# Optimization experiments

Hardware: AMD Instinct MI355X
Metric: run time of the kernel (lower is better)

## Reference

```python
import jax, jax.numpy as jnp
import numpy as np

D_MODEL = 512
HEADS = 8
D_FF = 1024
EPS = 1e-5


def layer_norm(x, gamma, beta):
    mu = jnp.mean(x, axis=-1, keepdims=True)
    var = jnp.mean(jnp.square(x - mu), axis=-1, keepdims=True)
    return (x - mu) * jax.lax.rsqrt(var + EPS) * gamma + beta


def mha(q, k, v, mask=None):
    # q,k,v: [B, S, D]; no input/output projections in the original module
    B, Sq, D = q.shape
    Sk = k.shape[1]
    dk = D // HEADS
    qh = q.reshape(B, Sq, HEADS, dk).transpose(0, 2, 1, 3)  # [B,H,Sq,dk]
    kh = k.reshape(B, Sk, HEADS, dk).transpose(0, 2, 1, 3)
    vh = v.reshape(B, Sk, HEADS, dk).transpose(0, 2, 1, 3)
    scores = jnp.einsum('bhqd,bhkd->bhqk', qh, kh) / np.sqrt(dk).astype(q.dtype)
    if mask is not None:
        scores = jnp.where(mask == 0, jnp.asarray(-1e9, scores.dtype), scores)
    attn = jax.nn.softmax(scores, axis=-1)  # dropout is identity in eval mode
    out = jnp.einsum('bhqk,bhkd->bhqd', attn, vh)
    return out.transpose(0, 2, 1, 3).reshape(B, Sq, D)


def setup_inputs() -> dict:
    key = jax.random.key(0)
    ks = jax.random.split(key, 8)
    B, S = 4, 2048
    x = jax.random.normal(ks[0], (B, S, D_MODEL), dtype=jnp.float32)
    encoder_output = jax.random.normal(ks[1], (B, S, D_MODEL), dtype=jnp.float32)
    mask = jax.random.randint(ks[2], (B, 1, S, S), 0, 2, dtype=jnp.int32)
    params = {
        'ln1_g': jnp.ones((D_MODEL,), jnp.float32), 'ln1_b': jnp.zeros((D_MODEL,), jnp.float32),
        'ln2_g': jnp.ones((D_MODEL,), jnp.float32), 'ln2_b': jnp.zeros((D_MODEL,), jnp.float32),
        'ln3_g': jnp.ones((D_MODEL,), jnp.float32), 'ln3_b': jnp.zeros((D_MODEL,), jnp.float32),
        'W1': jax.random.normal(ks[3], (D_MODEL, D_FF), jnp.float32) * (1.0 / np.sqrt(D_MODEL)),
        'b1': jnp.zeros((D_FF,), jnp.float32),
        'W2': jax.random.normal(ks[4], (D_FF, D_MODEL), jnp.float32) * (1.0 / np.sqrt(D_FF)),
        'b2': jnp.zeros((D_MODEL,), jnp.float32),
    }
    return {'x': x, 'encoder_output': encoder_output, 'mask': mask, **params}


def reference(x, encoder_output, mask, ln1_g, ln1_b, ln2_g, ln2_b, ln3_g, ln3_b, W1, b1, W2, b2):
    # pre-norm masked self-attention + residual (dropout = identity, eval mode)
    x1 = layer_norm(x, ln1_g, ln1_b)
    x = x + mha(x1, x1, x1, mask)
    # pre-norm cross-attention + residual
    x1 = layer_norm(x, ln2_g, ln2_b)
    x = x + mha(x1, encoder_output, encoder_output, None)
    # pre-norm FFN + residual
    x1 = layer_norm(x, ln3_g, ln3_b)
    h = jax.nn.relu(x1 @ W1 + b1)
    x = x + (h @ W2 + b2)
    return x
```

## Files before the change

### kernel.cpp

```cpp
#include <hip/hip_runtime.h>
#include <hip/hip_bf16.h>

#define D_MODEL 512
#define HEADS   8
#define DK      64
#define D_FF    1024
#define SEQ     2048
#define BATCH   4
#define NTOK    (BATCH*SEQ)
#define NELEM   (NTOK*D_MODEL)

#define QSCALE  0.18033688011112042f
#define MFIX    40.0f

typedef __attribute__((ext_vector_type(8))) short bf8_t;
typedef __attribute__((ext_vector_type(4))) short bf4_t;
typedef __attribute__((ext_vector_type(4))) float f4_t;

#define GLD16(gp, lp) __builtin_amdgcn_global_load_lds( \
    (const __attribute__((address_space(1))) void*)(gp), \
    (__attribute__((address_space(3))) void*)(lp), 16, 0, 0)

__device__ __forceinline__ float ldf(const void* p, size_t i, int f32) {
    return f32 ? ((const float*)p)[i] : __bfloat162float(((const __hip_bfloat16*)p)[i]);
}
__device__ __forceinline__ short f2bf(float f) {
    union { __hip_bfloat16 h; short s; } u; u.h = __float2bfloat16(f); return u.s;
}
__device__ __forceinline__ float bf2f(short s) {
    return __uint_as_float(((unsigned)(unsigned short)s) << 16);
}
__device__ __forceinline__ unsigned fbits(float f) { return __float_as_uint(f); }

__device__ __forceinline__ float fast_exp2(float x) {
    float r; asm("v_exp_f32 %0, %1" : "=v"(r) : "v"(x)); return r;
}

__global__ void detect_k(const uint4* __restrict__ w, int* __restrict__ flags) {
    __shared__ int found;
    if (threadIdx.x == 0) found = 0;
    __syncthreads();
    int hit = 0;
    for (int i = threadIdx.x; i < 4096; i += 256) {
        uint4 u = w[i];
        if (((u.x & 0x7F80u) == 0x7F80u) || ((u.y & 0x7F80u) == 0x7F80u) ||
            ((u.z & 0x7F80u) == 0x7F80u) || ((u.w & 0x7F80u) == 0x7F80u)) hit = 1;
    }
    if (hit) atomicOr(&found, 1);
    __syncthreads();
    if (threadIdx.x == 0) flags[0] = found ? 1 : 0;
}

__device__ __forceinline__ void transpose_body(const void* src, __hip_bfloat16* dst,
                                               int K, int N, int bxi, int byi, int f32,
                                               __hip_bfloat16 (*t)[33]) {
    int bx = bxi * 32, by = byi * 32;
    int tx = threadIdx.x & 31, ty = threadIdx.x >> 5;
    #pragma unroll
    for (int j = 0; j < 32; j += 8)
        t[ty + j][tx] = __float2bfloat16(ldf(src, (size_t)(by + ty + j) * N + bx + tx, f32));
    __syncthreads();
    #pragma unroll
    for (int j = 0; j < 32; j += 8)
        dst[(size_t)(bx + ty + j) * K + by + tx] = t[tx][ty + j];
}

__global__ __launch_bounds__(256)
void prep_k(const void* __restrict__ enc, const int* __restrict__ mask,
            const void* __restrict__ W1, const void* __restrict__ W2,
            const void* __restrict__ x,
            const void* __restrict__ ln1g, const void* __restrict__ ln1b,
            const void* __restrict__ ln2g, const void* __restrict__ ln2b,
            const void* __restrict__ ln3g, const void* __restrict__ ln3b,
            const void* __restrict__ b1,   const void* __restrict__ b2,
            const int* __restrict__ flagp,
            __hip_bfloat16* __restrict__ bufE, unsigned* __restrict__ mb,
            __hip_bfloat16* __restrict__ W1T, __hip_bfloat16* __restrict__ W2T,
            float* __restrict__ bufX, __hip_bfloat16* __restrict__ bufQ,
            __hip_bfloat16* __restrict__ pbuf) {
    __shared__ __hip_bfloat16 t[32][33];
    int f32 = *flagp;
    int bid = blockIdx.x;
    if (bid < 4096) {
        int i = bid * 256 + threadIdx.x;
        if (f32) {
            float4 a = ((const float4*)enc)[i];
            bf4_t o = { f2bf(a.x), f2bf(a.y), f2bf(a.z), f2bf(a.w) };
            ((bf4_t*)bufE)[i] = o;
        } else {
            ((bf4_t*)bufE)[i] = ((const bf4_t*)enc)[i];
        }
    } else if (bid < 6144) {
        int row  = (bid - 4096) * 4 + (threadIdx.x >> 6);
        int lane = threadIdx.x & 63;
        const int* mr = mask + (size_t)row * SEQ;
        for (int it = 0; it < SEQ/64; it++) {
            unsigned long long bal = __ballot(mr[it*64 + lane] != 0);
            if (lane == 0)  mb[(size_t)row*(SEQ/32) + it*2]     = (unsigned)bal;
            if (lane == 32) mb[(size_t)row*(SEQ/32) + it*2 + 1] = (unsigned)(bal >> 32);
        }
    } else if (bid < 6656) {
        int lb = bid - 6144;
        transpose_body(W1, W1T, D_MODEL, D_FF, lb & 31, lb >> 5, f32, t);
    } else if (bid < 7168) {
        int lb = bid - 6656;
        transpose_body(W2, W2T, D_FF, D_MODEL, lb & 15, lb >> 4, f32, t);
    } else if (bid < 9216) {
        int row  = (bid - 7168) * 4 + (threadIdx.x >> 6);
        int lane = threadIdx.x & 63;
        size_t base = (size_t)row * D_MODEL;
        float v[8];
        if (f32) {
            const float4* xp = (const float4*)((const float*)x + base);
            float4 a = xp[lane], b4 = xp[64 + lane];
            v[0]=a.x; v[1]=a.y; v[2]=a.z; v[3]=a.w;
            v[4]=b4.x; v[5]=b4.y; v[6]=b4.z; v[7]=b4.w;
        } else {
            const bf4_t* xp = (const bf4_t*)((const __hip_bfloat16*)x + base);
            bf4_t a = xp[lane], b4 = xp[64 + lane];
            v[0]=bf2f(a[0]); v[1]=bf2f(a[1]); v[2]=bf2f(a[2]); v[3]=bf2f(a[3]);
            v[4]=bf2f(b4[0]); v[5]=bf2f(b4[1]); v[6]=bf2f(b4[2]); v[7]=bf2f(b4[3]);
        }
        float s = 0.f;
        #pragma unroll
        for (int i = 0; i < 8; i++) s += v[i];
        #pragma unroll
        for (int off = 32; off; off >>= 1) s += __shfl_xor(s, off);
        float mu = s * (1.f / D_MODEL);
        float ss = 0.f;
        #pragma unroll
        for (int i = 0; i < 8; i++) { float d = v[i] - mu; ss += d * d; }
        #pragma unroll
        for (int off = 32; off; off >>= 1) ss += __shfl_xor(ss, off);
        float rstd = rsqrtf(ss * (1.f / D_MODEL) + 1e-5f);
        int c0 = 4*lane, c1 = 256 + 4*lane;
        ((float4*)(bufX + base))[lane]      = make_float4(v[0], v[1], v[2], v[3]);
        ((float4*)(bufX + base))[64 + lane] = make_float4(v[4], v[5], v[6], v[7]);
        bf4_t qa, qb;
        #pragma unroll
        for (int j = 0; j < 4; j++) {
            qa[j] = f2bf((v[j]   - mu) * rstd * ldf(ln1g, c0 + j, f32) + ldf(ln1b, c0 + j, f32));
            qb[j] = f2bf((v[4+j] - mu) * rstd * ldf(ln1g, c1 + j, f32) + ldf(ln1b, c1 + j, f32));
        }
        ((bf4_t*)(bufQ + base))[lane]      = qa;
        ((bf4_t*)(bufQ + base))[64 + lane] = qb;
    } else {
        int i = threadIdx.x;
        for (int k = i; k < 512; k += 256) {
            pbuf[k]        = __float2bfloat16(ldf(ln2g, k, f32));
            pbuf[512 + k]  = __float2bfloat16(ldf(ln2b, k, f32));
            pbuf[1024 + k] = __float2bfloat16(ldf(ln3g, k, f32));
            pbuf[1536 + k] = __float2bfloat16(ldf(ln3b, k, f32));
            pbuf[3072 + k] = __float2bfloat16(ldf(b2, k, f32));
        }
        for (int k = i; k < 1024; k += 256)
            pbuf[2048 + k] = __float2bfloat16(ldf(b1, k, f32));
    }
}

__global__ __launch_bounds__(256)
void layernorm_k(const float* __restrict__ x, const __hip_bfloat16* __restrict__ g,
                 const __hip_bfloat16* __restrict__ b,
                 __hip_bfloat16* __restrict__ y) {
    int row  = blockIdx.x * 4 + (threadIdx.x >> 6);
    int lane = threadIdx.x & 63;
    const float4* xp = (const float4*)(x + (size_t)row * D_MODEL);
    float4 a = xp[lane], b4 = xp[64 + lane];
    float v[8] = {a.x, a.y, a.z, a.w, b4.x, b4.y, b4.z, b4.w};
    float s = 0.f;
    #pragma unroll
    for (int i = 0; i < 8; i++) s += v[i];
    #pragma unroll
    for (int off = 32; off; off >>= 1) s += __shfl_xor(s, off);
    float mu = s * (1.f / D_MODEL);
    float ss = 0.f;
    #pragma unroll
    for (int i = 0; i < 8; i++) { float d = v[i] - mu; ss += d * d; }
    #pragma unroll
    for (int off = 32; off; off >>= 1) ss += __shfl_xor(ss, off);
    float rstd = rsqrtf(ss * (1.f / D_MODEL) + 1e-5f);
    bf4_t ga = ((const bf4_t*)g)[lane], gb = ((const bf4_t*)g)[64 + lane];
    bf4_t ba = ((const bf4_t*)b)[lane], bb = ((const bf4_t*)b)[64 + lane];
    bf4_t ya, yb;
    #pragma unroll
    for (int j = 0; j < 4; j++) {
        ya[j] = f2bf((v[j]   - mu) * rstd * bf2f(ga[j]) + bf2f(ba[j]));
        yb[j] = f2bf((v[4+j] - mu) * rstd * bf2f(gb[j]) + bf2f(bb[j]));
    }
    ((bf4_t*)(y + (size_t)row * D_MODEL))[lane]      = ya;
    ((bf4_t*)(y + (size_t)row * D_MODEL))[64 + lane] = yb;
}

__device__ __forceinline__ bf8_t prescale_q(bf8_t q) {
    bf8_t r;
    #pragma unroll
    for (int j = 0; j < 8; j++) r[j] = f2bf(bf2f(q[j]) * QSCALE);
    return r;
}

template<bool HAS_MASK>
__global__ __launch_bounds__(256, 2)
void attn_mfma_k(const __hip_bfloat16* __restrict__ Q, const __hip_bfloat16* __restrict__ K,
                 const __hip_bfloat16* __restrict__ V, const unsigned* __restrict__ mbits,
                 float* __restrict__ Xout) {
    int bid0 = blockIdx.x;
    int bid = ((bid0 & 7) << 6) | (bid0 >> 3);
    int qt = bid & 15;
    int h  = (bid >> 4) & 7;
    int b  = bid >> 7;
    int q0 = qt * 128;
    int tid  = threadIdx.x;
    int w    = tid >> 6;
    int lane = tid & 63;
    int c    = lane & 15;
    int quad = lane >> 4;

    __shared__ __hip_bfloat16 Kt[4][64 * 64];
    __shared__ __hip_bfloat16 VT[4][64 * 64];
    __shared__ __hip_bfloat16 Pb[4][2][16 * 64];

    bf8_t qf[2][2];
    #pragma unroll
    for (int g = 0; g < 2; g++) {
        const __hip_bfloat16* qrp = Q + ((size_t)(b*SEQ + q0 + 32*w + 16*g + c)) * D_MODEL + h*DK;
        qf[g][0] = prescale_q(*(const bf8_t*)(qrp + quad*8));
        qf[g][1] = prescale_q(*(const bf8_t*)(qrp + 32 + quad*8));
    }

    int kpo[4][2], vpo[4][2];
    #pragma unroll
    for (int t = 0; t < 4; t++)
        #pragma unroll
        for (int kh = 0; kh < 2; kh++) {
            int row = 16*t + c;
            kpo[t][kh] = (row*64 + (((4*kh + quad) ^ (row & 7)) * 8)) * 2;
            vpo[t][kh] = (row*64 + (((4*kh + quad) ^ (row & 7) ^ ((row >> 3) & 7)) * 8)) * 2;
        }

    int key0 = (tid >> 3) * 2, d0 = (tid & 7) * 8;
    int vtwo[8];
    #pragma unroll
    for (int j = 0; j < 8; j++) {
        int dk = d0 + j;
        int ch = (key0 >> 3) ^ (dk & 7) ^ ((dk >> 3) & 7);
        vtwo[j] = dk*128 + ch*16 + (key0 & 7)*2;
    }

    int krow[2], kc8[2];
    #pragma unroll
    for (int i = 0; i < 2; i++) {
        int idx = i*256 + tid;
        krow[i] = idx >> 3;
        kc8[i]  = ((idx & 7) ^ (krow[i] & 7)) * 8;
    }

    char* pbw[2] = { (char*)&Pb[w][0][0], (char*)&Pb[w][1][0] };
    int pwoff[4], proff[2];
    #pragma unroll
    for (int nt = 0; nt < 4; nt++)
        pwoff[nt] = c*128 + (((2*nt + (quad >> 1)) ^ (c & 7)) * 16) + (quad & 1)*8;
    #pragma unroll
    for (int kh = 0; kh < 2; kh++)
        proff[kh] = c*128 + (((4*kh + quad) ^ (c & 7)) * 16);

    const unsigned* mrp[2] = {nullptr, nullptr};
    if (HAS_MASK) {
        mrp[0] = mbits + (size_t)(b*SEQ + q0 + 32*w + c) * (SEQ/32);
        mrp[1] = mrp[0] + (size_t)16 * (SEQ/32);
    }
    int qsh = quad * 4;

    short onev = (c == 0) ? (short)0x3F80 : (short)0;
    bf8_t ones = {onev, onev, onev, onev, onev, onev, onev, onev};

    f4_t o[2][4];
    #pragma unroll
    for (int g = 0; g < 2; g++)
        #pragma unroll
        for (int mt = 0; mt < 4; mt++) o[g][mt] = (f4_t){0.f,0.f,0.f,0.f};
    f4_t l_acc[2] = {(f4_t){0.f,0.f,0.f,0.f}, (f4_t){0.f,0.f,0.f,0.f}};

    const size_t kvbase = (size_t)b * SEQ * D_MODEL + (size_t)h * DK;

    auto loadV = [&](int k0, bf8_t (&r0)[2], bf8_t (&r1)[2]) {
        #pragma unroll
        for (int t = 0; t < 2; t++) {
            const __hip_bfloat16* Vg = V + kvbase + (size_t)(k0 + t*64 + key0) * D_MODEL + d0;
            r0[t] = *(const bf8_t*)Vg;
            r1[t] = *(const bf8_t*)(Vg + D_MODEL);
        }
    };
    auto stageK = [&](int k0, int bufbase) {
        #pragma unroll
        for (int t = 0; t < 2; t++) {
            const __hip_bfloat16* Kg = K + kvbase + (size_t)(k0 + t*64) * D_MODEL;
            GLD16(Kg + (size_t)krow[0]*D_MODEL + kc8[0], (char*)&Kt[bufbase + t][0] + (w*64) * 16);
            GLD16(Kg + (size_t)krow[1]*D_MODEL + kc8[1], (char*)&Kt[bufbase + t][0] + (256 + w*64) * 16);
        }
    };
    auto writeV = [&](const bf8_t (&r0)[2], const bf8_t (&r1)[2], int bufbase) {
        #pragma unroll
        for (int t = 0; t < 2; t++) {
            const unsigned* v0u = (const unsigned*)&r0[t];
            const unsigned* v1u = (const unsigned*)&r1[t];
            char* vb = (char*)&VT[bufbase + t][0];
            #pragma unroll
            for (int dw = 0; dw < 4; dw++) {
                *(unsigned*)(vb + vtwo[2*dw])     = __builtin_amdgcn_perm(v1u[dw], v0u[dw], 0x05040100u);
                *(unsigned*)(vb + vtwo[2*dw + 1]) = __builtin_amdgcn_perm(v1u[dw], v0u[dw], 0x07060302u);
            }
        }
    };

    uint4 pm[2];
    if (HAS_MASK) { pm[0] = *(const uint4*)(mrp[0]); pm[1] = *(const uint4*)(mrp[1]); }
    bf8_t cv0[2], cv1[2];
    loadV(0, cv0, cv1);
    stageK(0, 0);
    writeV(cv0, cv1, 0);
    __syncthreads();

    for (int ph = 0; ph < SEQ/128; ph++) {
        int pb = (ph & 1) ? 2 : 0;
        int nb = pb ^ 2;

        uint4 nm[2];
        bf8_t nv0[2], nv1[2];
        if (ph < SEQ/128 - 1) {
            int kn = (ph + 1) * 128;
            if (HAS_MASK) {
                nm[0] = *(const uint4*)(mrp[0] + (kn >> 5));
                nm[1] = *(const uint4*)(mrp[1] + (kn >> 5));
            }
            loadV(kn, nv0, nv1);
            stageK(kn, nb);
        }

        #pragma unroll
        for (int t = 0; t < 2; t++) {
            const char* ktb = (const char*)&Kt[pb + t][0];
            const char* vtb = (const char*)&VT[pb + t][0];

            f4_t s[2][4];
            #pragma unroll
            for (int nt = 0; nt < 4; nt++) {
                s[0][nt] = (f4_t){-MFIX,-MFIX,-MFIX,-MFIX};
                s[1][nt] = (f4_t){-MFIX,-MFIX,-MFIX,-MFIX};
            }
            __builtin_amdgcn_s_setprio(1);
            #pragma unroll
            for (int nt = 0; nt < 4; nt++)
                #pragma unroll
                for (int kh = 0; kh < 2; kh++) {
                    bf8_t kf = *(const bf8_t*)(ktb + kpo[nt][kh]);
                    s[0][nt] = __builtin_amdgcn_mfma_f32_16x16x32_bf16(kf, qf[0][kh], s[0][nt], 0, 0, 0);
                    s[1][nt] = __builtin_amdgcn_mfma_f32_16x16x32_bf16(kf, qf[1][kh], s[1][nt], 0, 0, 0);
                }
            __builtin_amdgcn_s_setprio(0);

            #pragma unroll
            for (int g = 0; g < 2; g++) {
                unsigned wq0 = 0xffffffffu, wq1 = 0xffffffffu;
                if (HAS_MASK) {
                    wq0 = (t ? pm[g].z : pm[g].x) >> qsh;
                    wq1 = (t ? pm[g].w : pm[g].y) >> qsh;
                }
                #pragma unroll
                for (int nt = 0; nt < 4; nt++) {
                    #pragma unroll
                    for (int r = 0; r < 4; r++) {
                        float p = fast_exp2(s[g][nt][r]);
                        if (HAS_MASK) {
                            unsigned sel = (nt < 2) ? wq0 : wq1;
                            if (!((sel >> ((nt & 1)*16 + r)) & 1u)) p = 0.f;
                        }
                        s[g][nt][r] = p;
                    }
                    unsigned pk0 = __builtin_amdgcn_perm(fbits(s[g][nt][1]), fbits(s[g][nt][0]), 0x07060302u);
                    unsigned pk1 = __builtin_amdgcn_perm(fbits(s[g][nt][3]), fbits(s[g][nt][2]), 0x07060302u);
                    *(uint2*)(pbw[g] + pwoff[nt]) = make_uint2(pk0, pk1);
                }
            }

            __builtin_amdgcn_s_setprio(1);
            #pragma unroll
            for (int kh = 0; kh < 2; kh++) {
                bf8_t pfA = *(const bf8_t*)(pbw[0] + proff[kh]);
                bf8_t pfB = *(const bf8_t*)(pbw[1] + proff[kh]);
                l_acc[0] = __builtin_amdgcn_mfma_f32_16x16x32_bf16(ones, pfA, l_acc[0], 0, 0, 0);
                l_acc[1] = __builtin_amdgcn_mfma_f32_16x16x32_bf16(ones, pfB, l_acc[1], 0, 0, 0);
                #pragma unroll
                for (int mt = 0; mt < 4; mt++) {
                    bf8_t vf = *(const bf8_t*)(vtb + vpo[mt][kh]);
                    o[0][mt] = __builtin_amdgcn_mfma_f32_16x16x32_bf16(vf, pfA, o[0][mt], 0, 0, 0);
                    o[1][mt] = __builtin_amdgcn_mfma_f32_16x16x32_bf16(vf, pfB, o[1][mt], 0, 0, 0);
                }
            }
            __builtin_amdgcn_s_setprio(0);
        }

        if (ph < SEQ/128 - 1) {
            writeV(nv0, nv1, nb);
            if (HAS_MASK) { pm[0] = nm[0]; pm[1] = nm[1]; }
        }
        __syncthreads();
    }

    #pragma unroll
    for (int g = 0; g < 2; g++) {
        float lq = __shfl(l_acc[g][0], c);
        float il = 1.f / fmaxf(lq, 1e-35f);
        size_t rb = ((size_t)(b*SEQ + q0 + 32*w + 16*g + c)) * D_MODEL + h*DK;
        #pragma unroll
        for (int mt = 0; mt < 4; mt++) {
            float4* xp = (float4*)(Xout + rb + 16*mt + quad*4);
            float4 x4 = *xp;
            x4.x += o[g][mt][0] * il;
            x4.y += o[g][mt][1] * il;
            x4.z += o[g][mt][2] * il;
            x4.w += o[g][mt][3] * il;
            *xp = x4;
        }
    }
}

__global__ __launch_bounds__(256, 2)
void gemm_relu_k(const __hip_bfloat16* __restrict__ A, const __hip_bfloat16* __restrict__ BT,
                 const __hip_bfloat16* __restrict__ bias,
                 __hip_bfloat16* __restrict__ C, int Ksz, int Nsz) {
    __shared__ __hip_bfloat16 As[2][128 * 64];
    __shared__ __hip_bfloat16 Bs[2][128 * 64];
    int tid  = threadIdx.x;
    int w    = tid >> 6;
    int c    = tid & 15;
    int quad = (tid >> 4) & 3;
    int wy = w >> 1, wx = w & 1;
    int lin = blockIdx.y * gridDim.x + blockIdx.x;
    int swz = ((lin & 7) << 6) | (lin >> 3);
    int r0 = (swz >> 3) * 128, c0 = (swz & 7) * 128;

    f4_t acc[4][4];
    #pragma unroll
    for (int i = 0; i < 4; i++)
        #pragma unroll
        for (int j = 0; j < 4; j++) acc[i][j] = (f4_t){0.f,0.f,0.f,0.f};

    auto stage = [&](int k0, int bi) {
        #pragma unroll
        for (int i = 0; i < 4; i++) {
            int idx = i*256 + tid;
            int row = idx >> 3, c8 = idx & 7;
            GLD16(A  + (size_t)(r0 + row) * Ksz + k0 + ((c8 ^ (row & 7)) * 8),
                  (char*)&As[bi][0] + (size_t)(i*256 + w*64) * 16);
            GLD16(BT + (size_t)(c0 + row) * Ksz + k0 + ((c8 ^ (row & 7)) * 8),
                  (char*)&Bs[bi][0] + (size_t)(i*256 + w*64) * 16);
        }
    };

    stage(0, 0);
    __syncthreads();
    int nk = Ksz >> 6;
    for (int ks = 0; ks < nk; ks++) {
        int bi = ks & 1;
        if (ks + 1 < nk) stage((ks + 1) << 6, bi ^ 1);

        #pragma unroll
        for (int kh = 0; kh < 2; kh++) {
            bf8_t af[4], bf[4];
            #pragma unroll
            for (int mt = 0; mt < 4; mt++) {
                int row = wy*64 + mt*16 + c;
                af[mt] = *(const bf8_t*)&As[bi][row*64 + (((kh*4 + quad) ^ (row & 7)) * 8)];
            }
            #pragma unroll
            for (int nt = 0; nt < 4; nt++) {
                int row = wx*64 + nt*16 + c;
                bf[nt] = *(const bf8_t*)&Bs[bi][row*64 + (((kh*4 + quad) ^ (row & 7)) * 8)];
            }
            #pragma unroll
            for (int mt = 0; mt < 4; mt++)
                #pragma unroll
                for (int nt = 0; nt < 4; nt++)
                    acc[mt][nt] = __builtin_amdgcn_mfma_f32_16x16x32_bf16(af[mt], bf[nt], acc[mt][nt], 0, 0, 0);
        }
        __syncthreads();
    }

    #pragma unroll
    for (int mt = 0; mt < 4; mt++)
        #pragma unroll
        for (int nt = 0; nt < 4; nt++) {
            int col = c0 + wx*64 + nt*16 + c;
            float bv = __bfloat162float(bias[col]);
            #pragma unroll
            for (int r = 0; r < 4; r++) {
                int m = r0 + wy*64 + mt*16 + quad*4 + r;
                C[(size_t)m * Nsz + col] = __float2bfloat16(fmaxf(acc[mt][nt][r] + bv, 0.f));
            }
        }
}

__global__ __launch_bounds__(256, 2)
void gemm_out_k(const __hip_bfloat16* __restrict__ A, const __hip_bfloat16* __restrict__ BT,
                const __hip_bfloat16* __restrict__ bias, const float* __restrict__ resid,
                const int* __restrict__ flagp, void* __restrict__ out, int Ksz, int Nsz) {
    int f32 = *flagp;
    __shared__ __hip_bfloat16 As[2][128 * 64];
    __shared__ __hip_bfloat16 Bs[2][64 * 64];
    int tid  = threadIdx.x;
    int w    = tid >> 6;
    int c    = tid & 15;
    int quad = (tid >> 4) & 3;
    int lin = blockIdx.y * gridDim.x + blockIdx.x;
    int swz = ((lin & 7) << 6) | (lin >> 3);
    int r0 = (swz >> 3) * 128, c0 = (swz & 7) * 64;

    f4_t acc[2][4];
    #pragma unroll
    for (int i = 0; i < 2; i++)
        #pragma unroll
        for (int j = 0; j < 4; j++) acc[i][j] = (f4_t){0.f,0.f,0.f,0.f};

    auto stage = [&](int k0, int bi) {
        #pragma unroll
        for (int i = 0; i < 4; i++) {
            int idx = i*256 + tid;
            int row = idx >> 3, c8 = idx & 7;
            GLD16(A + (size_t)(r0 + row) * Ksz + k0 + ((c8 ^ (row & 7)) * 8),
                  (char*)&As[bi][0] + (size_t)(i*256 + w*64) * 16);
        }
        #pragma unroll
        for (int i = 0; i < 2; i++) {
            int idx = i*256 + tid;
            int row = idx >> 3, c8 = idx & 7;
            GLD16(BT + (size_t)(c0 + row) * Ksz + k0 + ((c8 ^ (row & 7)) * 8),
                  (char*)&Bs[bi][0] + (size_t)(i*256 + w*64) * 16);
        }
    };

    stage(0, 0);
    __syncthreads();
    int nk = Ksz >> 6;
    for (int ks = 0; ks < nk; ks++) {
        int bi = ks & 1;
        if (ks + 1 < nk) stage((ks + 1) << 6, bi ^ 1);

        #pragma unroll
        for (int kh = 0; kh < 2; kh++) {
            bf8_t af[2], bf[4];
            #pragma unroll
            for (int mt = 0; mt < 2; mt++) {
                int row = w*32 + mt*16 + c;
                af[mt] = *(const bf8_t*)&As[bi][row*64 + (((kh*4 + quad) ^ (row & 7)) * 8)];
            }
            #pragma unroll
            for (int nt = 0; nt < 4; nt++) {
                int row = nt*16 + c;
                bf[nt] = *(const bf8_t*)&Bs[bi][row*64 + (((kh*4 + quad) ^ (row & 7)) * 8)];
            }
            #pragma unroll
            for (int mt = 0; mt < 2; mt++)
                #pragma unroll
                for (int nt = 0; nt < 4; nt++)
                    acc[mt][nt] = __builtin_amdgcn_mfma_f32_16x16x32_bf16(af[mt], bf[nt], acc[mt][nt], 0, 0, 0);
        }
        __syncthreads();
    }

    #pragma unroll
    for (int mt = 0; mt < 2; mt++)
        #pragma unroll
        for (int nt = 0; nt < 4; nt++) {
            int col = c0 + nt*16 + c;
            float bv = __bfloat162float(bias[col]);
            #pragma unroll
            for (int r = 0; r < 4; r++) {
                int m = r0 + w*32 + mt*16 + quad*4 + r;
                float v = acc[mt][nt][r] + bv + resid[(size_t)m * Nsz + col];
                if (f32) ((float*)out)[(size_t)m * Nsz + col] = v;
                else     ((__hip_bfloat16*)out)[(size_t)m * Nsz + col] = __float2bfloat16(v);
            }
        }
}

extern "C" void kernel_launch(void* const* d_in, const int* in_sizes, int n_in,
                              void* d_out, int out_size, void* d_ws, size_t ws_size,
                              hipStream_t stream) {
    const void* x    = d_in[0];
    const void* enc  = d_in[1];
    const int*  mask = (const int*)d_in[2];
    const void* ln1g = d_in[3];
    const void* ln1b = d_in[4];
    const void* ln2g = d_in[5];
    const void* ln2b = d_in[6];
    const void* ln3g = d_in[7];
    const void* ln3b = d_in[8];
    const void* W1   = d_in[9];
    const void* b1   = d_in[10];
    const void* W2   = d_in[11];
    const void* b2   = d_in[12];

    char* ws = (char*)d_ws;
    float*          bufX  = (float*)ws;
    __hip_bfloat16* bufQ  = (__hip_bfloat16*)(ws + (16u<<20));
    __hip_bfloat16* bufE  = (__hip_bfloat16*)(ws + (24u<<20));
    __hip_bfloat16* bufH  = (__hip_bfloat16*)(ws + (32u<<20));
    __hip_bfloat16* W1T   = (__hip_bfloat16*)(ws + (48u<<20));
    __hip_bfloat16* W2T   = (__hip_bfloat16*)(ws + (49u<<20));
    unsigned*       mbits = (unsigned*)(ws + (50u<<20));
    int*            flags = (int*)(ws + (52u<<20));
    __hip_bfloat16* pbuf  = (__hip_bfloat16*)(ws + (52u<<20) + 4096);

    dim3 blk(256);
    detect_k<<<1, blk, 0, stream>>>((const uint4*)x, flags);
    prep_k<<<9217, blk, 0, stream>>>(enc, mask, W1, W2, x, ln1g, ln1b,
                                     ln2g, ln2b, ln3g, ln3b, b1, b2, flags,
                                     bufE, mbits, W1T, W2T, bufX, bufQ, pbuf);

    attn_mfma_k<true><<<BATCH*HEADS*(SEQ/128), blk, 0, stream>>>(bufQ, bufQ, bufQ, mbits, bufX);
    layernorm_k<<<NTOK/4, blk, 0, stream>>>(bufX, pbuf, pbuf + 512, bufQ);
    attn_mfma_k<false><<<BATCH*HEADS*(SEQ/128), blk, 0, stream>>>(bufQ, bufE, bufE, nullptr, bufX);
    layernorm_k<<<NTOK/4, blk, 0, stream>>>(bufX, pbuf + 1024, pbuf + 1536, bufQ);
    gemm_relu_k<<<dim3(D_FF/128, NTOK/128), blk, 0, stream>>>(bufQ, W1T, pbuf + 2048, bufH, D_MODEL, D_FF);
    gemm_out_k<<<dim3(D_MODEL/64, NTOK/128), blk, 0, stream>>>(bufH, W2T, pbuf + 3072, bufX, flags, d_out, D_FF, D_MODEL);
}
```

Before: 330.3 us.

## Double attention query tile to 256 rows with 512-thread blocks sharing K/V

The attention kernel now processes 256 query rows per block using 8 waves instead of 128 rows with 4 waves. Each K/V tile staged in LDS is reused by twice as many waves, which halves global K/V traffic and per-block staging work per thread. The cost is half as many blocks (256 instead of 512), possibly lower occupancy with launch bounds of 512 threads at 2 blocks/CU, and a larger probability-scratch LDS allocation.

```diff
diff --git a/kernel.cpp b/kernel.cpp
--- a/kernel.cpp
+++ b/kernel.cpp
@@ -199,16 +199,16 @@
 }
 
 template<bool HAS_MASK>
-__global__ __launch_bounds__(256, 2)
+__global__ __launch_bounds__(512, 2)
 void attn_mfma_k(const __hip_bfloat16* __restrict__ Q, const __hip_bfloat16* __restrict__ K,
                  const __hip_bfloat16* __restrict__ V, const unsigned* __restrict__ mbits,
                  float* __restrict__ Xout) {
     int bid0 = blockIdx.x;
-    int bid = ((bid0 & 7) << 6) | (bid0 >> 3);
-    int qt = bid & 15;
-    int h  = (bid >> 4) & 7;
-    int b  = bid >> 7;
-    int q0 = qt * 128;
+    int bid = ((bid0 & 7) << 5) | (bid0 >> 3);
+    int qt = bid & 7;
+    int h  = (bid >> 3) & 7;
+    int b  = bid >> 6;
+    int q0 = qt * 256;
     int tid  = threadIdx.x;
     int w    = tid >> 6;
     int lane = tid & 63;
@@ -217,7 +217,7 @@
 
     __shared__ __hip_bfloat16 Kt[4][64 * 64];
     __shared__ __hip_bfloat16 VT[4][64 * 64];
-    __shared__ __hip_bfloat16 Pb[4][2][16 * 64];
+    __shared__ __hip_bfloat16 Pb[8][2][16 * 64];
 
     bf8_t qf[2][2];
     #pragma unroll
@@ -237,7 +237,8 @@
             vpo[t][kh] = (row*64 + (((4*kh + quad) ^ (row & 7) ^ ((row >> 3) & 7)) * 8)) * 2;
         }
 
-    int key0 = (tid >> 3) * 2, d0 = (tid & 7) * 8;
+    int vtile = tid >> 8;
+    int key0 = ((tid & 255) >> 3) * 2, d0 = (tid & 7) * 8;
     int vtwo[8];
     #pragma unroll
     for (int j = 0; j < 8; j++) {
@@ -246,13 +247,8 @@
         vtwo[j] = dk*128 + ch*16 + (key0 & 7)*2;
     }
 
-    int krow[2], kc8[2];
-    #pragma unroll
-    for (int i = 0; i < 2; i++) {
-        int idx = i*256 + tid;
-        krow[i] = idx >> 3;
-        kc8[i]  = ((idx & 7) ^ (krow[i] & 7)) * 8;
-    }
+    int krow = tid >> 3;
+    int kc8  = ((tid & 7) ^ (krow & 7)) * 8;
 
     char* pbw[2] = { (char*)&Pb[w][0][0], (char*)&Pb[w][1][0] };
     int pwoff[4], proff[2];
@@ -282,39 +278,32 @@
 
     const size_t kvbase = (size_t)b * SEQ * D_MODEL + (size_t)h * DK;
 
-    auto loadV = [&](int k0, bf8_t (&r0)[2], bf8_t (&r1)[2]) {
-        #pragma unroll
-        for (int t = 0; t < 2; t++) {
-            const __hip_bfloat16* Vg = V + kvbase + (size_t)(k0 + t*64 + key0) * D_MODEL + d0;
-            r0[t] = *(const bf8_t*)Vg;
-            r1[t] = *(const bf8_t*)(Vg + D_MODEL);
-        }
+    auto loadV = [&](int k0, bf8_t& r0, bf8_t& r1) {
+        const __hip_bfloat16* Vg = V + kvbase + (size_t)(k0 + vtile*64 + key0) * D_MODEL + d0;
+        r0 = *(const bf8_t*)Vg;
+        r1 = *(const bf8_t*)(Vg + D_MODEL);
     };
     auto stageK = [&](int k0, int bufbase) {
         #pragma unroll
         for (int t = 0; t < 2; t++) {
             const __hip_bfloat16* Kg = K + kvbase + (size_t)(k0 + t*64) * D_MODEL;
-            GLD16(Kg + (size_t)krow[0]*D_MODEL + kc8[0], (char*)&Kt[bufbase + t][0] + (w*64) * 16);
-            GLD16(Kg + (size_t)krow[1]*D_MODEL + kc8[1], (char*)&Kt[bufbase + t][0] + (256 + w*64) * 16);
+            GLD16(Kg + (size_t)krow*D_MODEL + kc8, (char*)&Kt[bufbase + t][0] + (w*64) * 16);
         }
     };
-    auto writeV = [&](const bf8_t (&r0)[2], const bf8_t (&r1)[2], int bufbase) {
-        #pragma unroll
-        for (int t = 0; t < 2; t++) {
-            const unsigned* v0u = (const unsigned*)&r0[t];
-            const unsigned* v1u = (const unsigned*)&r1[t];
-            char* vb = (char*)&VT[bufbase + t][0];
-            #pragma unroll
-            for (int dw = 0; dw < 4; dw++) {
-                *(unsigned*)(vb + vtwo[2*dw])     = __builtin_amdgcn_perm(v1u[dw], v0u[dw], 0x05040100u);
-                *(unsigned*)(vb + vtwo[2*dw + 1]) = __builtin_amdgcn_perm(v1u[dw], v0u[dw], 0x07060302u);
-            }
+    auto writeV = [&](const bf8_t& r0, const bf8_t& r1, int bufbase) {
+        const unsigned* v0u = (const unsigned*)&r0;
+        const unsigned* v1u = (const unsigned*)&r1;
+        char* vb = (char*)&VT[bufbase + vtile][0];
+        #pragma unroll
+        for (int dw = 0; dw < 4; dw++) {
+            *(unsigned*)(vb + vtwo[2*dw])     = __builtin_amdgcn_perm(v1u[dw], v0u[dw], 0x05040100u);
+            *(unsigned*)(vb + vtwo[2*dw + 1]) = __builtin_amdgcn_perm(v1u[dw], v0u[dw], 0x07060302u);
         }
     };
 
     uint4 pm[2];
     if (HAS_MASK) { pm[0] = *(const uint4*)(mrp[0]); pm[1] = *(const uint4*)(mrp[1]); }
-    bf8_t cv0[2], cv1[2];
+    bf8_t cv0, cv1;
     loadV(0, cv0, cv1);
     stageK(0, 0);
     writeV(cv0, cv1, 0);
@@ -325,7 +314,7 @@
         int nb = pb ^ 2;
 
         uint4 nm[2];
-        bf8_t nv0[2], nv1[2];
+        bf8_t nv0, nv1;
         if (ph < SEQ/128 - 1) {
             int kn = (ph + 1) * 128;
             if (HAS_MASK) {
@@ -612,14 +601,15 @@
     __hip_bfloat16* pbuf  = (__hip_bfloat16*)(ws + (52u<<20) + 4096);
 
     dim3 blk(256);
+    dim3 ablk(512);
     detect_k<<<1, blk, 0, stream>>>((const uint4*)x, flags);
     prep_k<<<9217, blk, 0, stream>>>(enc, mask, W1, W2, x, ln1g, ln1b,
                                      ln2g, ln2b, ln3g, ln3b, b1, b2, flags,
                                      bufE, mbits, W1T, W2T, bufX, bufQ, pbuf);
 
-    attn_mfma_k<true><<<BATCH*HEADS*(SEQ/128), blk, 0, stream>>>(bufQ, bufQ, bufQ, mbits, bufX);
+    attn_mfma_k<true><<<BATCH*HEADS*(SEQ/256), ablk, 0, stream>>>(bufQ, bufQ, bufQ, mbits, bufX);
     layernorm_k<<<NTOK/4, blk, 0, stream>>>(bufX, pbuf, pbuf + 512, bufQ);
-    attn_mfma_k<false><<<BATCH*HEADS*(SEQ/128), blk, 0, stream>>>(bufQ, bufE, bufE, nullptr, bufX);
+    attn_mfma_k<false><<<BATCH*HEADS*(SEQ/256), ablk, 0, stream>>>(bufQ, bufE, bufE, nullptr, bufX);
     layernorm_k<<<NTOK/4, blk, 0, stream>>>(bufX, pbuf + 1024, pbuf + 1536, bufQ);
     gemm_relu_k<<<dim3(D_FF/128, NTOK/128), blk, 0, stream>>>(bufQ, W1T, pbuf + 2048, bufH, D_MODEL, D_FF);
     gemm_out_k<<<dim3(D_MODEL/64, NTOK/128), blk, 0, stream>>>(bufH, W2T, pbuf + 3072, bufX, flags, d_out, D_FF, D_MODEL);
```

New measurement: 326.2 us, median of 2. No clear change (-1.2%).
